# Performance work log

Measured on AMD Instinct MI355X. Metric: run time of the kernel, lower is better.

## Reference

```python
import jax, jax.numpy as jnp
import numpy as np

EPS_W = 1e-5  # weight floor added before normalization
EPS_D = 1e-5  # denom floor in inverse-CDF interpolation


def sample_pdf(bins, weights, n_samp):
    """Inverse-CDF importance sampling (deterministic, det=True).
    bins: [N, M+1], weights: [N, M] -> samples: [N, n_samp].
    Replaces the torch O(M) comparison loop with a per-ray binary search
    (jnp.searchsorted side='right' over the first M cdf entries), which
    computes the exact same index: above = #{i in [0,M): u >= cdf[i]}."""
    N, M = weights.shape
    w = weights + EPS_W
    pdf = w / jnp.sum(w, axis=-1, keepdims=True)
    cdf = jnp.cumsum(pdf, axis=-1)
    cdf = jnp.concatenate([jnp.zeros_like(cdf[:, :1]), cdf], axis=-1)  # [N, M+1]
    u = jnp.broadcast_to(jnp.linspace(0.0, 1.0, n_samp, dtype=bins.dtype), (N, n_samp))
    above = jax.vmap(lambda c, uu: jnp.searchsorted(c, uu, side='right'))(cdf[:, :M], u)
    below = jnp.clip(above - 1, 0)
    cdf_b = jnp.take_along_axis(cdf, below, axis=-1)
    cdf_a = jnp.take_along_axis(cdf, above, axis=-1)
    bins_b = jnp.take_along_axis(bins, below, axis=-1)
    bins_a = jnp.take_along_axis(bins, above, axis=-1)
    denom = cdf_a - cdf_b
    denom = jnp.where(denom < EPS_D, jnp.ones_like(denom), denom)
    t = (u - cdf_b) / denom
    return bins_b + t * (bins_a - bins_b)


def setup_inputs() -> dict:
    key = jax.random.key(0)
    k0, k1, k2, k3 = jax.random.split(key, 4)
    N, Np = 65536, 64
    rays_o = jax.random.normal(k0, (N, 3), dtype=jnp.float32) * 0.1
    rd = jax.random.normal(k1, (N, 3), dtype=jnp.float32)
    rays_d = rd / jnp.linalg.norm(rd, axis=-1, keepdims=True)
    # sorted per-ray depths in [near=2, far=6]
    z_vals = jnp.sort(jax.random.uniform(k2, (N, Np), dtype=jnp.float32,
                                         minval=2.0, maxval=6.0), axis=-1)
    weights = jax.random.uniform(k3, (N, Np), dtype=jnp.float32)
    return {"rays_o": rays_o, "rays_d": rays_d, "weights": weights,
            "z_vals": z_vals, "N_importance": 64}


def reference(rays_o, rays_d, weights, z_vals, N_importance):
    """Faithful jax version of sample_fine_pts (det=True, inv_uniform=False)."""
    Np = z_vals.shape[1]
    z_mid = 0.5 * (z_vals[:, 1:] + z_vals[:, :-1])        # [N, Np-1] bins
    w_mid = weights[:, 1:-1]                              # [N, Np-2]
    z_samples = sample_pdf(z_mid, w_mid, N_importance)    # [N, N_importance]
    z_all = jnp.sort(jnp.concatenate([z_vals, z_samples], axis=-1), axis=-1)
    # pts = z * d + o  -> [N, Np+N_importance, 3]
    pts = z_all[:, :, None] * rays_d[:, None, :] + rays_o[:, None, :]
    return pts, z_all
```

## Files before the change

### kernel.cpp

```cpp
#include <hip/hip_runtime.h>

#define NP 64
#define M  62
#define RPB 4

__global__ __launch_bounds__(256) void nerf_fine_kernel(
    const float* __restrict__ rays_o,
    const float* __restrict__ rays_d,
    const float* __restrict__ weights,
    const float* __restrict__ z_vals,
    float* __restrict__ pts,
    float* __restrict__ z_all_out,
    int N)
{
    const int lane = threadIdx.x & 63;
    const int w    = threadIdx.x >> 6;
    const int ray  = blockIdx.x * RPB + w;
    if (ray >= N) return;

    const float zv  = z_vals [(size_t)ray * NP + lane];
    const float wt  = weights[(size_t)ray * NP + lane];
    const float rd0 = rays_d[(size_t)ray * 3 + 0];
    const float rd1 = rays_d[(size_t)ray * 3 + 1];
    const float rd2 = rays_d[(size_t)ray * 3 + 2];
    const float ro0 = rays_o[(size_t)ray * 3 + 0];
    const float ro1 = rays_o[(size_t)ray * 3 + 1];
    const float ro2 = rays_o[(size_t)ray * 3 + 2];

    const float binsv = 0.5f * (zv + __shfl_down(zv, 1));

    float v = __shfl_down(wt, 1) + 1e-5f;
    v = (lane < M) ? v : 0.0f;
    #pragma unroll
    for (int off = 1; off < 64; off <<= 1) {
        float t = __shfl_up(v, off);
        if (lane >= off) v += t;
    }
    const float rtot = __builtin_amdgcn_rcpf(__shfl(v, 63));
    const float cdfv = v * rtot;

    const float u = (float)lane * (1.0f / 63.0f);
    int lo = 0, hi = M;
    #pragma unroll
    for (int it = 0; it < 6; ++it) {
        const int mid = (lo + hi) >> 1;
        float cv = __shfl(cdfv, mid - 1);
        cv = (mid == 0) ? -1.0f : cv;
        const bool le  = (cv <= u);
        const bool act = lo < hi;
        lo = (act &&  le) ? mid + 1 : lo;
        hi = (act && !le) ? mid     : hi;
    }
    const int above = lo;
    const int below = above - 1;
    const float ca = __shfl(cdfv, above - 1);
    float cb = __shfl(cdfv, below - 1);
    cb = (below == 0) ? 0.0f : cb;
    const float bb = __shfl(binsv, below);
    const float ba = __shfl(binsv, above);
    float denom = ca - cb;
    denom = (denom < 1e-5f) ? 1.0f : denom;
    const float t  = (u - cb) * __builtin_amdgcn_rcpf(denom);
    const float zs = fmaf(t, ba - bb, bb);

    float lov, hiv;
    {
        const float t0 = __shfl_xor(zs, 63);
        lov = fminf(zv, t0);
        hiv = fmaxf(zv, t0);
        #pragma unroll
        for (int d = 32; d >= 1; d >>= 1) {
            const float pl = __shfl_xor(lov, d);
            const float ph = __shfl_xor(hiv, d);
            const bool up  = (lane & d) != 0;
            lov = up ? fmaxf(lov, pl) : fminf(lov, pl);
            hiv = up ? fmaxf(hiv, ph) : fminf(hiv, ph);
        }
    }

    float* zo = z_all_out + (size_t)ray * 128;
    zo[lane]      = lov;
    zo[64 + lane] = hiv;

    const int i0 = (2 * lane)     & 63;
    const int i1 = (2 * lane + 1) & 63;
    const float gl0 = __shfl(lov, i0), gh0 = __shfl(hiv, i0);
    const float gl1 = __shfl(lov, i1), gh1 = __shfl(hiv, i1);
    const float zA = (lane < 32) ? gl0 : gh0;
    const float zB = (lane < 32) ? gl1 : gh1;

    float2* p2 = (float2*)(pts + (size_t)ray * 384 + 6 * lane);
    float2 q0, q1, q2;
    q0.x = fmaf(zA, rd0, ro0);  q0.y = fmaf(zA, rd1, ro1);
    q1.x = fmaf(zA, rd2, ro2);  q1.y = fmaf(zB, rd0, ro0);
    q2.x = fmaf(zB, rd1, ro1);  q2.y = fmaf(zB, rd2, ro2);
    p2[0] = q0;
    p2[1] = q1;
    p2[2] = q2;
}

extern "C" void kernel_launch(void* const* d_in, const int* in_sizes, int n_in,
                              void* d_out, int out_size, void* d_ws, size_t ws_size,
                              hipStream_t stream) {
    const float* rays_o  = (const float*)d_in[0];
    const float* rays_d  = (const float*)d_in[1];
    const float* weights = (const float*)d_in[2];
    const float* z_vals  = (const float*)d_in[3];

    const int N = in_sizes[2] / NP;
    float* pts   = (float*)d_out;
    float* z_all = (float*)d_out + (size_t)N * 128 * 3;

    const int blocks = (N + RPB - 1) / RPB;
    nerf_fine_kernel<<<blocks, 256, 0, stream>>>(rays_o, rays_d, weights, z_vals,
                                                 pts, z_all, N);
}
```

Baseline: 34.64 us.

## Use DPP row scan, shifted loads, and direct scalar pts stores

Replaces the shuffle-based prefix scan with a DPP row_shr plus row_bcast scan and a readlane for the total. The shifted z/weight values now come from a second global load at lane+1 instead of cross-lane shuffles. The output stage drops the four gathering shuffles and writes pts as six strided scalar stores per lane instead of three float2 stores. The aim is to remove the LDS/bpermute shuffle latency, at the cost of extra loads and less coalesced stores.

```diff
diff --git a/kernel.cpp b/kernel.cpp
--- a/kernel.cpp
+++ b/kernel.cpp
@@ -3,6 +3,12 @@
 #define NP 64
 #define M  62
 #define RPB 4
+
+template<int CTRL, int RM>
+__device__ __forceinline__ float dpp_add(float x) {
+    const int y = __builtin_amdgcn_update_dpp(0, __float_as_int(x), CTRL, RM, 0xF, true);
+    return x + __int_as_float(y);
+}
 
 __global__ __launch_bounds__(256) void nerf_fine_kernel(
     const float* __restrict__ rays_o,
@@ -18,8 +24,11 @@
     const int ray  = blockIdx.x * RPB + w;
     if (ray >= N) return;
 
+    const int lp1 = (lane < 63) ? (lane + 1) : 63;
     const float zv  = z_vals [(size_t)ray * NP + lane];
-    const float wt  = weights[(size_t)ray * NP + lane];
+    const float zsh = z_vals [(size_t)ray * NP + lp1];
+    const float wsh = weights[(size_t)ray * NP + lp1];
+
     const float rd0 = rays_d[(size_t)ray * 3 + 0];
     const float rd1 = rays_d[(size_t)ray * 3 + 1];
     const float rd2 = rays_d[(size_t)ray * 3 + 2];
@@ -27,17 +36,20 @@
     const float ro1 = rays_o[(size_t)ray * 3 + 1];
     const float ro2 = rays_o[(size_t)ray * 3 + 2];
 
-    const float binsv = 0.5f * (zv + __shfl_down(zv, 1));
+    const float binsv = 0.5f * (zv + zsh);
 
-    float v = __shfl_down(wt, 1) + 1e-5f;
-    v = (lane < M) ? v : 0.0f;
-    #pragma unroll
-    for (int off = 1; off < 64; off <<= 1) {
-        float t = __shfl_up(v, off);
-        if (lane >= off) v += t;
-    }
-    const float rtot = __builtin_amdgcn_rcpf(__shfl(v, 63));
-    const float cdfv = v * rtot;
+    float v = (lane < M) ? (wsh + 1e-5f) : 0.0f;
+
+    v = dpp_add<0x111, 0xF>(v);
+    v = dpp_add<0x112, 0xF>(v);
+    v = dpp_add<0x114, 0xF>(v);
+    v = dpp_add<0x118, 0xF>(v);
+    v = dpp_add<0x142, 0xA>(v);
+    v = dpp_add<0x143, 0xC>(v);
+
+    const float total = __int_as_float(__builtin_amdgcn_readlane(__float_as_int(v), 63));
+    const float rtot  = __builtin_amdgcn_rcpf(total);
+    const float cdfv  = v * rtot;
 
     const float u = (float)lane * (1.0f / 63.0f);
     int lo = 0, hi = M;
@@ -82,21 +94,13 @@
     zo[lane]      = lov;
     zo[64 + lane] = hiv;
 
-    const int i0 = (2 * lane)     & 63;
-    const int i1 = (2 * lane + 1) & 63;
-    const float gl0 = __shfl(lov, i0), gh0 = __shfl(hiv, i0);
-    const float gl1 = __shfl(lov, i1), gh1 = __shfl(hiv, i1);
-    const float zA = (lane < 32) ? gl0 : gh0;
-    const float zB = (lane < 32) ? gl1 : gh1;
-
-    float2* p2 = (float2*)(pts + (size_t)ray * 384 + 6 * lane);
-    float2 q0, q1, q2;
-    q0.x = fmaf(zA, rd0, ro0);  q0.y = fmaf(zA, rd1, ro1);
-    q1.x = fmaf(zA, rd2, ro2);  q1.y = fmaf(zB, rd0, ro0);
-    q2.x = fmaf(zB, rd1, ro1);  q2.y = fmaf(zB, rd2, ro2);
-    p2[0] = q0;
-    p2[1] = q1;
-    p2[2] = q2;
+    float* pp = pts + (size_t)ray * 384 + 3 * lane;
+    pp[0]   = fmaf(lov, rd0, ro0);
+    pp[1]   = fmaf(lov, rd1, ro1);
+    pp[2]   = fmaf(lov, rd2, ro2);
+    pp[192] = fmaf(hiv, rd0, ro0);
+    pp[193] = fmaf(hiv, rd1, ro1);
+    pp[194] = fmaf(hiv, rd2, ro2);
 }
 
 extern "C" void kernel_launch(void* const* d_in, const int* in_sizes, int n_in,
```

New measurement: 32.04 us. -7.5%, faster.
